# Kernel tuning notes

Hardware: AMD Instinct MI355X
Metric: run time of the kernel (lower is better)

The kernel has to match this reference:

```python
import jax, jax.numpy as jnp
import numpy as np

HARD_RATIO = 0.5
HARD_WEIGHT = 0.5
B, Q, D = 1024, 32, 512


def _l2norm(x):
    return x / jnp.linalg.norm(x, axis=-1, keepdims=True)


def setup_inputs() -> dict:
    key = jax.random.key(0)
    k1, k2 = jax.random.split(key)
    fusion_feats = _l2norm(jax.random.normal(k1, (B, D), dtype=jnp.float32))
    target_feats = _l2norm(jax.random.normal(k2, (B, Q, D), dtype=jnp.float32))
    temp = jnp.float32(0.07)
    return {"fusion_feats": fusion_feats, "target_feats": target_feats, "temp": temp}


def reference(fusion_feats, target_feats, temp):
    b = fusion_feats.shape[0]
    # sim[i, j, q] = fusion[i] . target[j, q]  -> max over query tokens q
    sim = jnp.einsum('id,jqd->ijq', fusion_feats, target_feats)  # (B, B, Q)
    sim_max = jnp.max(sim, axis=-1) / temp                        # (B, B)

    # standard InfoNCE with diagonal labels
    loss_standard = -jnp.mean(jnp.diagonal(jax.nn.log_softmax(sim_max, axis=-1)))

    # online hard-negative mining: per-row top-k over off-diagonal entries
    num_hard = max(1, int(b * HARD_RATIO))
    diag_mask = jnp.eye(b, dtype=bool)
    masked = jnp.where(diag_mask, -jnp.inf, sim_max)
    hard_sims, _ = jax.lax.top_k(masked, num_hard)                # (B, num_hard)
    pos = jnp.diagonal(sim_max)                                    # (B,)
    # -log(exp(pos) / (exp(pos) + sum exp(hard))) = logsumexp([pos, hard]) - pos
    lse = jax.nn.logsumexp(jnp.concatenate([pos[:, None], hard_sims], axis=1), axis=1)
    hard_loss_online = jnp.mean(lse - pos)

    total_loss = loss_standard + HARD_WEIGHT * hard_loss_online
    return total_loss
```

## Files before the change

kernel.cpp:

```cpp
#include <hip/hip_runtime.h>
#include <hip/hip_bf16.h>
#include <math.h>

typedef unsigned short u16;
typedef unsigned char u8;
typedef unsigned int u32;
typedef long long i64;
typedef __attribute__((ext_vector_type(4))) float f32x4;

__global__ void cvt_fused(const float* __restrict__ F, const float* __restrict__ T,
                          u32* __restrict__ Fb, u32* __restrict__ Tb,
                          float* __restrict__ out) {
    const int idx = blockIdx.x * blockDim.x + threadIdx.x;
    if (idx == 0) out[0] = 0.f;
    const float* s;
    u32* d;
    int i;
    if (idx < 65536) { s = F; d = Fb; i = idx; }
    else             { s = T; d = Tb; i = idx - 65536; }
    const float4 v0 = *(const float4*)(s + (size_t)i * 8);
    const float4 v1 = *(const float4*)(s + (size_t)i * 8 + 4);
    int lo = __builtin_amdgcn_cvt_pk_fp8_f32(v0.x * 16.f, v0.y * 16.f, 0, false);
    lo     = __builtin_amdgcn_cvt_pk_fp8_f32(v0.z * 16.f, v0.w * 16.f, lo, true);
    int hi = __builtin_amdgcn_cvt_pk_fp8_f32(v1.x * 16.f, v1.y * 16.f, 0, false);
    hi     = __builtin_amdgcn_cvt_pk_fp8_f32(v1.z * 16.f, v1.w * 16.f, hi, true);
    uint2 o; o.x = (u32)lo; o.y = (u32)hi;
    const int r  = i >> 6;
    const int ob = (i & 63) << 3;
    const int t  = ob >> 7;
    const int ss = (ob >> 5) & 3;
    const int f  = (ob >> 3) & 3;
    const int o2 = (t << 7) | (f << 5) | (ss << 3);
    ((uint2*)d)[r * 64 + (o2 >> 3)] = o;
}

#define GLB_AS __attribute__((address_space(1)))
#define LDS_AS __attribute__((address_space(3)))

__device__ __forceinline__ void gload_lds16(const void* g, void* l) {
    __builtin_amdgcn_global_load_lds((const GLB_AS void*)g, (LDS_AS void*)l, 16, 0, 0);
}

__device__ __forceinline__ i64 half0(int4 v) { int2 p; p.x = v.x; p.y = v.y; return __builtin_bit_cast(i64, p); }
__device__ __forceinline__ i64 half1(int4 v) { int2 p; p.x = v.z; p.y = v.w; return __builtin_bit_cast(i64, p); }

__global__ __launch_bounds__(256, 4)
void gemm_max(const u8* __restrict__ A, const u8* __restrict__ B,
              const float* __restrict__ temp_ptr, float* __restrict__ sim) {
    __shared__ __align__(16) u8 lA[64 * 128];
    __shared__ __align__(16) u8 lB[128 * 128];
    const int bn = blockIdx.x;
    const int bm = blockIdx.y;
    const int tid  = threadIdx.x;
    const int wave = tid >> 6;
    const int lane = tid & 63;
    const int wm = wave >> 1;
    const int wn = wave & 1;

    f32x4 acc[2][4] = {};

    const int srow = lane >> 3;
    const int aoff = srow * 512 + (((lane & 7) ^ srow) << 4);
    const u8* gA = A + (size_t)(bm * 64)  * 512 + aoff;
    const u8* gB = B + (size_t)(bn * 128) * 512 + aoff;

    const int frow = lane & 15;
    const int fq   = lane >> 4;
    const int r7   = frow & 7;

    for (int k0 = 0; k0 < 512; k0 += 128) {
        gload_lds16(gA + (wave)     * 4096 + k0, lA + (wave)     * 1024);
        gload_lds16(gA + (wave + 4) * 4096 + k0, lA + (wave + 4) * 1024);
#pragma unroll
        for (int j = 0; j < 4; ++j)
            gload_lds16(gB + (wave + 4 * j) * 4096 + k0, lB + (wave + 4 * j) * 1024);
        __syncthreads();

#pragma unroll
        for (int sp = 0; sp < 2; ++sp) {
            const int coff = (((fq << 1) + sp) ^ r7) << 4;
            int4 aF[2], bF[4];
#pragma unroll
            for (int mt = 0; mt < 2; ++mt)
                aF[mt] = *(const int4*)&lA[(wm * 32 + mt * 16 + frow) * 128 + coff];
#pragma unroll
            for (int nt = 0; nt < 4; ++nt)
                bF[nt] = *(const int4*)&lB[(wn * 64 + nt * 16 + frow) * 128 + coff];
#pragma unroll
            for (int mt = 0; mt < 2; ++mt)
#pragma unroll
                for (int nt = 0; nt < 4; ++nt) {
                    acc[mt][nt] = __builtin_amdgcn_mfma_f32_16x16x32_fp8_fp8(
                        half0(aF[mt]), half0(bF[nt]), acc[mt][nt], 0, 0, 0);
                    acc[mt][nt] = __builtin_amdgcn_mfma_f32_16x16x32_fp8_fp8(
                        half1(aF[mt]), half1(bF[nt]), acc[mt][nt], 0, 0, 0);
                }
        }
        __syncthreads();
    }

    const float inv = 1.0f / (256.0f * (*temp_ptr));
    const int jb = (bn * 128 + wn * 64) >> 5;
#pragma unroll
    for (int mt = 0; mt < 2; ++mt) {
#pragma unroll
        for (int rr = 0; rr < 4; ++rr) {
            float v0 = fmaxf(acc[mt][0][rr], acc[mt][1][rr]);
            float v1 = fmaxf(acc[mt][2][rr], acc[mt][3][rr]);
#pragma unroll
            for (int off = 1; off < 16; off <<= 1) {
                v0 = fmaxf(v0, __shfl_xor(v0, off));
                v1 = fmaxf(v1, __shfl_xor(v1, off));
            }
            if ((lane & 15) == 0) {
                const int row = bm * 64 + wm * 32 + mt * 16 + fq * 4 + rr;
                sim[row * 1024 + jb]     = v0 * inv;
                sim[row * 1024 + jb + 1] = v1 * inv;
            }
        }
    }
}

__device__ __forceinline__ u32 f2key(float x) {
    u32 b = __float_as_uint(x);
    return (b & 0x80000000u) ? ~b : (b | 0x80000000u);
}
__device__ __forceinline__ float key2f(u32 k) {
    return __uint_as_float((k & 0x80000000u) ? (k & 0x7fffffffu) : ~k);
}

__global__ __launch_bounds__(256)
void row_loss(const float* __restrict__ sim, float* __restrict__ out) {
    const int tid = threadIdx.x;
    const int lane = tid & 63;
    const int wv = tid >> 6;
    const int i = blockIdx.x * 4 + wv;

    float v[16];
    const float4* rp = (const float4*)(sim + (size_t)i * 1024);
#pragma unroll
    for (int t = 0; t < 4; ++t) {
        float4 f = rp[t * 64 + lane];
        v[t * 4 + 0] = f.x; v[t * 4 + 1] = f.y; v[t * 4 + 2] = f.z; v[t * 4 + 3] = f.w;
    }

    const int dslot = ((i >> 8) << 2) | (i & 3);
    const int dlane = (i >> 2) & 63;

    u32 k[16];
#pragma unroll
    for (int t = 0; t < 16; ++t) {
        u32 kk = f2key(v[t]);
        k[t] = (lane == dlane && t == dslot) ? 0u : kk;
    }

    float pv = 0.f;
#pragma unroll
    for (int t = 0; t < 16; ++t) if (t == dslot) pv = v[t];
    const float pos = __shfl(pv, dlane);

    float m = v[0];
#pragma unroll
    for (int t = 1; t < 16; ++t) m = fmaxf(m, v[t]);
#pragma unroll
    for (int off = 32; off > 0; off >>= 1) m = fmaxf(m, __shfl_xor(m, off));
    float s = 0.f;
#pragma unroll
    for (int t = 0; t < 16; ++t) s += __expf(v[t] - m);
#pragma unroll
    for (int off = 32; off > 0; off >>= 1) s += __shfl_xor(s, off);
    const float loss_std = m + __logf(s) - pos;

    u32 lo = 0u, hi = 0xFFFFFFFFu;
    while (lo < hi) {
        const u32 span = hi - lo;
        const u32 mid = lo + (span >> 1) + (span & 1u);
        int cnt = 0;
#pragma unroll
        for (int t = 0; t < 16; ++t) cnt += (k[t] >= mid);
#pragma unroll
        for (int off = 32; off > 0; off >>= 1) cnt += __shfl_xor(cnt, off);
        if (cnt >= 512) lo = mid; else hi = mid - 1;
    }
    const u32 t_key = lo;
    const float tval = key2f(t_key);

    float se = 0.f;
    int cgt = 0;
#pragma unroll
    for (int t = 0; t < 16; ++t) {
        if (k[t] > t_key) { se += __expf(v[t] - m); ++cgt; }
    }
#pragma unroll
    for (int off = 32; off > 0; off >>= 1) se += __shfl_xor(se, off);
#pragma unroll
    for (int off = 32; off > 0; off >>= 1) cgt += __shfl_xor(cgt, off);

    const float sh = se + (float)(512 - cgt) * __expf(tval - m) + __expf(pos - m);
    const float hard = m + __logf(sh) - pos;

    if (lane == 0)
        atomicAdd(out, (loss_std + 0.5f * hard) * (1.0f / 1024.0f));
}

extern "C" void kernel_launch(void* const* d_in, const int* in_sizes, int n_in,
                              void* d_out, int out_size, void* d_ws, size_t ws_size,
                              hipStream_t stream) {
    const float* F    = (const float*)d_in[0];
    const float* T    = (const float*)d_in[1];
    const float* temp = (const float*)d_in[2];
    float* out = (float*)d_out;

    char* ws = (char*)d_ws;
    u32*  Fb8 = (u32*)ws;
    u32*  Tb8 = (u32*)(ws + (1u << 20));
    float* sim = (float*)(ws + (1u << 20) + (32u << 20));

    cvt_fused<<<8448, 256, 0, stream>>>(F, T, Fb8, Tb8, out);

    dim3 grid(256, 16);
    gemm_max<<<grid, 256, 0, stream>>>((const u8*)Fb8, (const u8*)Tb8, temp, sim);

    row_loss<<<256, 256, 0, stream>>>(sim, out);
}
```

Measured before the change: 159.3 us.

## Double-buffer LDS tiles in fp8 GEMM and remap block indices

The GEMM-max kernel now keeps two LDS buffers for the A and B tiles. It issues the async global-to-LDS load for the next K-slice before computing on the current one, which drops one barrier per iteration. The 2D grid becomes a 1D grid with a swizzled mapping of block id to (bn, bm), which changes the order tiles are visited for cache locality. LDS use per block doubles, so the launch-bounds occupancy hint drops from 4 to 3 blocks per CU.

Result: slower. 163.4 us (+2.6%).

```diff
diff --git a/kernel.cpp b/kernel.cpp
--- a/kernel.cpp
+++ b/kernel.cpp
@@ -44,13 +44,14 @@
 __device__ __forceinline__ i64 half0(int4 v) { int2 p; p.x = v.x; p.y = v.y; return __builtin_bit_cast(i64, p); }
 __device__ __forceinline__ i64 half1(int4 v) { int2 p; p.x = v.z; p.y = v.w; return __builtin_bit_cast(i64, p); }
 
-__global__ __launch_bounds__(256, 4)
+__global__ __launch_bounds__(256, 3)
 void gemm_max(const u8* __restrict__ A, const u8* __restrict__ B,
               const float* __restrict__ temp_ptr, float* __restrict__ sim) {
-    __shared__ __align__(16) u8 lA[64 * 128];
-    __shared__ __align__(16) u8 lB[128 * 128];
-    const int bn = blockIdx.x;
-    const int bm = blockIdx.y;
+    __shared__ __align__(16) u8 lA[2][64 * 128];
+    __shared__ __align__(16) u8 lB[2][128 * 128];
+    const int bid = blockIdx.x;
+    const int bn  = ((bid & 7) << 5) | ((bid >> 3) & 31);
+    const int bm  = bid >> 8;
     const int tid  = threadIdx.x;
     const int wave = tid >> 6;
     const int lane = tid & 63;
@@ -68,24 +69,31 @@
     const int fq   = lane >> 4;
     const int r7   = frow & 7;
 
-    for (int k0 = 0; k0 < 512; k0 += 128) {
-        gload_lds16(gA + (wave)     * 4096 + k0, lA + (wave)     * 1024);
-        gload_lds16(gA + (wave + 4) * 4096 + k0, lA + (wave + 4) * 1024);
-#pragma unroll
-        for (int j = 0; j < 4; ++j)
-            gload_lds16(gB + (wave + 4 * j) * 4096 + k0, lB + (wave + 4 * j) * 1024);
+#define STAGE(pb, k0)                                                                   \
+    do {                                                                                \
+        gload_lds16(gA + (wave)     * 4096 + (k0), &lA[pb][(wave)     * 1024]);         \
+        gload_lds16(gA + (wave + 4) * 4096 + (k0), &lA[pb][(wave + 4) * 1024]);         \
+        _Pragma("unroll")                                                               \
+        for (int j = 0; j < 4; ++j)                                                     \
+            gload_lds16(gB + (wave + 4 * j) * 4096 + (k0), &lB[pb][(wave + 4 * j) * 1024]); \
+    } while (0)
+
+    STAGE(0, 0);
+#pragma unroll
+    for (int t = 0; t < 4; ++t) {
         __syncthreads();
-
+        if (t < 3) STAGE((t + 1) & 1, (t + 1) * 128);
+        const int pb = t & 1;
 #pragma unroll
         for (int sp = 0; sp < 2; ++sp) {
             const int coff = (((fq << 1) + sp) ^ r7) << 4;
             int4 aF[2], bF[4];
 #pragma unroll
             for (int mt = 0; mt < 2; ++mt)
-                aF[mt] = *(const int4*)&lA[(wm * 32 + mt * 16 + frow) * 128 + coff];
+                aF[mt] = *(const int4*)&lA[pb][(wm * 32 + mt * 16 + frow) * 128 + coff];
 #pragma unroll
             for (int nt = 0; nt < 4; ++nt)
-                bF[nt] = *(const int4*)&lB[(wn * 64 + nt * 16 + frow) * 128 + coff];
+                bF[nt] = *(const int4*)&lB[pb][(wn * 64 + nt * 16 + frow) * 128 + coff];
 #pragma unroll
             for (int mt = 0; mt < 2; ++mt)
 #pragma unroll
@@ -96,8 +104,8 @@
                         half1(aF[mt]), half1(bF[nt]), acc[mt][nt], 0, 0, 0);
                 }
         }
-        __syncthreads();
-    }
+    }
+#undef STAGE
 
     const float inv = 1.0f / (256.0f * (*temp_ptr));
     const int jb = (bn * 128 + wn * 64) >> 5;
@@ -218,8 +226,7 @@
 
     cvt_fused<<<8448, 256, 0, stream>>>(F, T, Fb8, Tb8, out);
 
-    dim3 grid(256, 16);
-    gemm_max<<<grid, 256, 0, stream>>>((const u8*)Fb8, (const u8*)Tb8, temp, sim);
+    gemm_max<<<4096, 256, 0, stream>>>((const u8*)Fb8, (const u8*)Tb8, temp, sim);
 
     row_loss<<<256, 256, 0, stream>>>(sim, out);
 }
```
